# Kernel optimization log

Measured on AMD Instinct MI355X. Metric: run time of the kernel, lower is better.

The kernel has to match this reference:

```python
import jax, jax.numpy as jnp
import numpy as np

N = 20000      # total nodes across the mini-batch of graphs
E = 320000     # edges (avg degree 16)
B = 16         # graphs in the batch
HEADS = 8
EPS_BN = 1e-5
NEG_SLOPE = 0.2


def _lin(k, fan_in, fan_out):
    return (jax.random.normal(k, (fan_in, fan_out), jnp.float32) / np.float32(np.sqrt(fan_in)))


def setup_inputs() -> dict:
    key = jax.random.key(0)
    ks = jax.random.split(key, 24)
    inp = {}
    inp["x"] = jax.random.normal(ks[0], (N, 3), jnp.float32)
    inp["edge_index"] = jax.random.randint(ks[1], (2, E), 0, N, dtype=jnp.int32)
    inp["batch"] = jnp.sort(jax.random.randint(ks[2], (N,), 0, B, dtype=jnp.int32))
    # GATConv params: lin weight [in, heads*out], att_src/att_dst [heads,out], bias [heads*out]
    dims = [(3, 16), (128, 32), (256, 64)]
    for i, (cin, cout) in enumerate(dims, start=1):
        base = 3 + 5 * i
        inp[f"W{i}"] = _lin(ks[base], cin, HEADS * cout)
        inp[f"as{i}"] = jax.random.normal(ks[base + 1], (HEADS, cout), jnp.float32) * 0.1
        inp[f"ad{i}"] = jax.random.normal(ks[base + 2], (HEADS, cout), jnp.float32) * 0.1
        inp[f"b{i}"] = jnp.zeros((HEADS * cout,), jnp.float32)
        inp[f"g{i}"] = jnp.ones((HEADS * cout,), jnp.float32)
        inp[f"be{i}"] = jnp.zeros((HEADS * cout,), jnp.float32)
    inp["fcW"] = _lin(ks[20], 512, 10)
    inp["fcb"] = jnp.zeros((10,), jnp.float32)
    return inp


def gat_layer(x, src, dst, W, a_s, a_d, bias, heads, out_ch):
    n = x.shape[0]
    h = (x @ W).reshape(n, heads, out_ch)              # [N,H,C]
    al_s = jnp.einsum('nhc,hc->nh', h, a_s)            # [N,H]
    al_d = jnp.einsum('nhc,hc->nh', h, a_d)
    e = jax.nn.leaky_relu(al_s[src] + al_d[dst], NEG_SLOPE)   # [E,H]
    m = jax.ops.segment_max(e, dst, num_segments=n)    # per-dst softmax (stable)
    e = jnp.exp(e - m[dst])
    denom = jax.ops.segment_sum(e, dst, num_segments=n)
    alpha = e / (denom[dst] + 1e-16)
    out = jax.ops.segment_sum(h[src] * alpha[:, :, None], dst, num_segments=n)
    return out.reshape(n, heads * out_ch) + bias


def bn_relu(x, g, b):
    mu = x.mean(0)
    var = x.var(0)  # biased, as torch BN uses for normalization
    return jax.nn.relu((x - mu) * jax.lax.rsqrt(var + EPS_BN) * g + b)


def reference(x, edge_index, batch, W1, as1, ad1, b1, g1, be1,
              W2, as2, ad2, b2, g2, be2, W3, as3, ad3, b3, g3, be3, fcW, fcb):
    n = x.shape[0]
    loops = jnp.arange(n, dtype=edge_index.dtype)
    src = jnp.concatenate([edge_index[0], loops])  # add_self_loops=True (PyG default)
    dst = jnp.concatenate([edge_index[1], loops])
    h = bn_relu(gat_layer(x, src, dst, W1, as1, ad1, b1, HEADS, 16), g1, be1)
    h = bn_relu(gat_layer(h, src, dst, W2, as2, ad2, b2, HEADS, 32), g2, be2)
    h = bn_relu(gat_layer(h, src, dst, W3, as3, ad3, b3, HEADS, 64), g3, be3)
    pooled = jax.ops.segment_max(h, batch, num_segments=B)  # global_max_pool
    return pooled @ fcW + fcb
```

## Files before the change

### kernel.cpp

```cpp
#include <hip/hip_runtime.h>
#include <hip/hip_bf16.h>

#define HEADS 8
#define EPS_BN 1e-5f
#define NEG_SLOPE 0.2f
#define BN_NB 256

typedef __attribute__((ext_vector_type(8))) short bf16x8;
typedef __attribute__((ext_vector_type(4))) float f32x4;

__device__ __forceinline__ float bf2f(unsigned short u) {
    return __uint_as_float(((unsigned int)u) << 16);
}

__device__ __forceinline__ unsigned short f2bf(float f) {
    __hip_bfloat16 b = __float2bfloat16(f);
    return *reinterpret_cast<unsigned short*>(&b);
}

__device__ __forceinline__ void gld_lds16(const ushort* g, ushort* l) {
    __builtin_amdgcn_global_load_lds(
        (const __attribute__((address_space(1))) unsigned int*)g,
        (__attribute__((address_space(3))) unsigned int*)l, 16, 0, 0);
}


__global__ void count_kernel(const int* __restrict__ ei, int E, int N, int* __restrict__ counts) {
    int i = blockIdx.x * blockDim.x + threadIdx.x;
    int total = E + N;
    if (i >= total) return;
    int d = (i < E) ? ei[E + i] : (i - E);
    atomicAdd(&counts[d], 1);
}

__global__ __launch_bounds__(1024) void scan_block_kernel(const int* __restrict__ counts,
                                                          int* __restrict__ offs,
                                                          int* __restrict__ part, int n) {
    __shared__ int tile[1024];
    int tid = threadIdx.x;
    int gid = blockIdx.x * 1024 + tid;
    int v = (gid < n) ? counts[gid] : 0;
    tile[tid] = v;
    __syncthreads();
    for (int off = 1; off < 1024; off <<= 1) {
        int t = (tid >= off) ? tile[tid - off] : 0;
        __syncthreads();
        tile[tid] += t;
        __syncthreads();
    }
    if (gid < n) offs[gid + 1] = tile[tid];
    if (tid == 1023) part[blockIdx.x] = tile[1023];
}

__global__ __launch_bounds__(1024) void scan_add_kernel(int* __restrict__ offs,
                                                        const int* __restrict__ part, int n) {
    __shared__ int base;
    if (threadIdx.x == 0) {
        int s = 0;
        for (int i = 0; i < (int)blockIdx.x; ++i) s += part[i];
        base = s;
    }
    __syncthreads();
    int gid = blockIdx.x * 1024 + threadIdx.x;
    if (gid < n) offs[gid + 1] += base;
    if (gid == 0) offs[0] = 0;
}

__global__ void scatter_kernel(const int* __restrict__ ei, int E, int N,
                               const int* __restrict__ offs, int* __restrict__ cursor,
                               int* __restrict__ csr_src) {
    int i = blockIdx.x * blockDim.x + threadIdx.x;
    int total = E + N;
    if (i >= total) return;
    int s, d;
    if (i < E) { s = ei[i]; d = ei[E + i]; } else { s = i - E; d = i - E; }
    int slot = atomicAdd(&cursor[d], 1);
    csr_src[offs[d] + slot] = s;
}


__global__ __launch_bounds__(256) void linear1_al_kernel(const float* __restrict__ x,
                                                         const float* __restrict__ W,
                                                         const float* __restrict__ a_s,
                                                         const float* __restrict__ a_d,
                                                         ushort* __restrict__ h,
                                                         float* __restrict__ als,
                                                         float* __restrict__ ald, int N) {
    int tid = threadIdx.x;
    int n = blockIdx.x * 2 + (tid >> 7);
    int f = tid & 127;
    if (n >= N) return;
    float acc = x[n * 3 + 0] * W[f] + x[n * 3 + 1] * W[128 + f] + x[n * 3 + 2] * W[256 + f];
    h[(size_t)n * 128 + f] = f2bf(acc);
    float s = acc * a_s[f];
    float ds = acc * a_d[f];
    s += __shfl_xor(s, 1);  ds += __shfl_xor(ds, 1);
    s += __shfl_xor(s, 2);  ds += __shfl_xor(ds, 2);
    s += __shfl_xor(s, 4);  ds += __shfl_xor(ds, 4);
    s += __shfl_xor(s, 8);  ds += __shfl_xor(ds, 8);
    if ((f & 15) == 0) {
        int head = f >> 4;
        als[n * 8 + head] = s;
        ald[n * 8 + head] = ds;
    }
}


__global__ __launch_bounds__(256) void transpose_both_kernel(const float* __restrict__ W2,
                                                             ushort* __restrict__ Wt2,
                                                             const float* __restrict__ W3,
                                                             ushort* __restrict__ Wt3) {
    __shared__ float t[32][33];
    int bid = blockIdx.x;
    const float* W; ushort* Wt; int K, Nc, b;
    if (bid < 32) { W = W2; Wt = Wt2; K = 128; Nc = 256; b = bid; }
    else          { W = W3; Wt = Wt3; K = 256; Nc = 512; b = bid - 32; }
    int nb = Nc / 32;
    int bx = b % nb, by = b / nb;
    int n0 = bx * 32, k0 = by * 32;
    int lx = threadIdx.x & 31, ly = threadIdx.x >> 5;
    for (int r = ly; r < 32; r += 8) t[r][lx] = W[(size_t)(k0 + r) * Nc + n0 + lx];
    __syncthreads();
    for (int r = ly; r < 32; r += 8) Wt[(size_t)(n0 + r) * K + k0 + lx] = f2bf(t[lx][r]);
}


template<int F>
__global__ void prep_kernel(const ushort4* __restrict__ xb, const float* __restrict__ scale,
                            const float* __restrict__ shift, ushort4* __restrict__ A, int n4) {
    int i = blockIdx.x * blockDim.x + threadIdx.x;
    if (i >= n4) return;
    ushort4 u = xb[i];
    int f = (i << 2) & (F - 1);
    float4 sc = *(const float4*)(scale + f);
    float4 sh = *(const float4*)(shift + f);
    ushort4 o;
    o.x = f2bf(fmaxf(bf2f(u.x) * sc.x + sh.x, 0.f));
    o.y = f2bf(fmaxf(bf2f(u.y) * sc.y + sh.y, 0.f));
    o.z = f2bf(fmaxf(bf2f(u.z) * sc.z + sh.z, 0.f));
    o.w = f2bf(fmaxf(bf2f(u.w) * sc.w + sh.w, 0.f));
    A[i] = o;
}


template<int K, int C>
__global__ __launch_bounds__(256) void mfma_gemm_kernel(const ushort* __restrict__ A,
                                                        const ushort* __restrict__ Bt,
                                                        ushort* __restrict__ Cout,
                                                        const float* __restrict__ a_s,
                                                        const float* __restrict__ a_d,
                                                        float* __restrict__ als,
                                                        float* __restrict__ ald,
                                                        int M, int Ncols) {
    __shared__ __align__(16) ushort lA[128 * 64];
    __shared__ __align__(16) ushort lB[128 * 64];
    int tid = threadIdx.x;
    int l = tid & 63, w = tid >> 6;
    int m0 = blockIdx.x * 128;
    int n0 = blockIdx.y * 128;
    int wm = w >> 1, wn = w & 1;
    f32x4 zero = {0.f, 0.f, 0.f, 0.f};
    f32x4 acc[4][4];
#pragma unroll
    for (int m = 0; m < 4; ++m)
#pragma unroll
        for (int n = 0; n < 4; ++n) acc[m][n] = zero;

#pragma unroll
    for (int k0 = 0; k0 < K; k0 += 64) {
        if (k0) __syncthreads();
#pragma unroll
        for (int i = 0; i < 4; ++i) {
            int idx = (w * 4 + i) * 64 + l;
            int row = idx >> 3, p = idx & 7;
            int gc = (p ^ (row & 7)) * 8;
            int ar = m0 + row; ar = (ar < M) ? ar : (M - 1);
            gld_lds16(A + (size_t)ar * K + k0 + gc, &lA[idx * 8]);
            gld_lds16(Bt + (size_t)(n0 + row) * K + k0 + gc, &lB[idx * 8]);
        }
        __syncthreads();
#pragma unroll
        for (int ks = 0; ks < 2; ++ks) {
            bf16x8 af[4], bfr[4];
#pragma unroll
            for (int m = 0; m < 4; ++m) {
                int row = wm * 64 + m * 16 + (l & 15);
                int cp = (ks * 4 + (l >> 4)) ^ (row & 7);
                af[m] = *(const bf16x8*)&lA[row * 64 + cp * 8];
            }
#pragma unroll
            for (int n = 0; n < 4; ++n) {
                int row = wn * 64 + n * 16 + (l & 15);
                int cp = (ks * 4 + (l >> 4)) ^ (row & 7);
                bfr[n] = *(const bf16x8*)&lB[row * 64 + cp * 8];
            }
#pragma unroll
            for (int m = 0; m < 4; ++m)
#pragma unroll
                for (int n = 0; n < 4; ++n)
                    acc[m][n] = __builtin_amdgcn_mfma_f32_16x16x32_bf16(af[m], bfr[n], acc[m][n], 0, 0, 0);
        }
    }
    int lr = (l >> 4) * 4, lc = l & 15;
#pragma unroll
    for (int m = 0; m < 4; ++m) {
#pragma unroll
        for (int q = 0; q < 4; ++q) {
            int r = m0 + wm * 64 + m * 16 + lr + q;
            if (r < M) {
#pragma unroll
                for (int n = 0; n < 4; ++n) {
                    int c = n0 + wn * 64 + n * 16 + lc;
                    Cout[(size_t)r * Ncols + c] = f2bf(acc[m][n][q]);
                }
            }
        }
    }
    constexpr int GRP = (C == 64) ? 4 : 2;
    constexpr int NGRP = 4 / GRP;
    float asv[4], adv[4];
#pragma unroll
    for (int n = 0; n < 4; ++n) {
        int cc = n0 + wn * 64 + n * 16 + lc;
        asv[n] = a_s[cc];
        adv[n] = a_d[cc];
    }
#pragma unroll
    for (int m = 0; m < 4; ++m) {
#pragma unroll
        for (int q = 0; q < 4; ++q) {
            int r = m0 + wm * 64 + m * 16 + lr + q;
#pragma unroll
            for (int gg = 0; gg < NGRP; ++gg) {
                float s = 0.f, ds = 0.f;
#pragma unroll
                for (int nn = 0; nn < GRP; ++nn) {
                    int n = gg * GRP + nn;
                    s += acc[m][n][q] * asv[n];
                    ds += acc[m][n][q] * adv[n];
                }
                s += __shfl_xor(s, 1);  ds += __shfl_xor(ds, 1);
                s += __shfl_xor(s, 2);  ds += __shfl_xor(ds, 2);
                s += __shfl_xor(s, 4);  ds += __shfl_xor(ds, 4);
                s += __shfl_xor(s, 8);  ds += __shfl_xor(ds, 8);
                if (lc == 0 && r < M) {
                    int head = (n0 + wn * 64 + gg * (GRP * 16)) / C;
                    als[r * 8 + head] = s;
                    ald[r * 8 + head] = ds;
                }
            }
        }
    }
}


template<int CPL>
__device__ __forceinline__ void gather_accum(const ushort* hp, float wt, float* acc) {
    unsigned int u[CPL / 2];
    if constexpr (CPL == 8) {
        uint4 v = *(const uint4*)hp; u[0] = v.x; u[1] = v.y; u[2] = v.z; u[3] = v.w;
    } else if constexpr (CPL == 4) {
        uint2 v = *(const uint2*)hp; u[0] = v.x; u[1] = v.y;
    } else {
        u[0] = *(const unsigned int*)hp;
    }
#pragma unroll
    for (int j = 0; j < CPL / 2; ++j) {
        acc[2 * j]     += wt * __uint_as_float(u[j] << 16);
        acc[2 * j + 1] += wt * __uint_as_float(u[j] & 0xffff0000u);
    }
}

template<int F, int C>
__global__ __launch_bounds__(256) void aggregate_kernel(const ushort* __restrict__ h,
                                                        const float* __restrict__ als,
                                                        const float* __restrict__ ald,
                                                        const int* __restrict__ offs,
                                                        const int* __restrict__ csr_src,
                                                        const float* __restrict__ bias,
                                                        ushort* __restrict__ outbf, int N) {
    constexpr int CPL = F / 64;
    int w = threadIdx.x >> 6, l = threadIdx.x & 63;
    int d = blockIdx.x * 4 + w;
    if (d >= N) return;
    int start = offs[d];
    int deg = offs[d + 1] - start;
    int hf = l >> 3;
    int hw = l & 7;
    int jslot = l >> 3;
    float aldw = ald[d * 8 + hw];

    float acc[CPL];
#pragma unroll
    for (int j = 0; j < CPL; ++j) acc[j] = 0.f;
    float dsum = 0.f;
    float mrun = -1e30f;

    int nfull = deg & ~7;
    for (int eb = 0; eb < nfull; eb += 8) {
        int sE = (l < 8) ? csr_src[start + eb + l] : 0;
        int smy = __shfl(sE, jslot);
        float v = als[smy * 8 + hw] + aldw;
        v = (v > 0.f) ? v : NEG_SLOPE * v;
        float bm = v;
        bm = fmaxf(bm, __shfl_xor(bm, 8));
        bm = fmaxf(bm, __shfl_xor(bm, 16));
        bm = fmaxf(bm, __shfl_xor(bm, 32));
        float mnew = fmaxf(mrun, bm);
        float rs = __expf(mrun - mnew);
        float pw = __expf(v - mnew);
        dsum = dsum * rs + pw;
        float rsg = __shfl(rs, hf);
#pragma unroll
        for (int j = 0; j < CPL; ++j) acc[j] *= rsg;
        mrun = mnew;
#pragma unroll
        for (int j = 0; j < 8; ++j) {
            int sj = __shfl(sE, j);
            float wt = __shfl(pw, (j << 3) + hf);
            gather_accum<CPL>(h + (size_t)sj * F + l * CPL, wt, acc);
        }
    }
    int rem = deg - nfull;
    if (rem) {
        int sE = (l < rem) ? csr_src[start + nfull + l] : 0;
        int smy = __shfl(sE, jslot);
        float v = -1e30f;
        if (jslot < rem) {
            v = als[smy * 8 + hw] + aldw;
            v = (v > 0.f) ? v : NEG_SLOPE * v;
        }
        float bm = v;
        bm = fmaxf(bm, __shfl_xor(bm, 8));
        bm = fmaxf(bm, __shfl_xor(bm, 16));
        bm = fmaxf(bm, __shfl_xor(bm, 32));
        float mnew = fmaxf(mrun, bm);
        float rs = __expf(mrun - mnew);
        float pw = __expf(v - mnew);
        dsum = dsum * rs + pw;
        float rsg = __shfl(rs, hf);
#pragma unroll
        for (int j = 0; j < CPL; ++j) acc[j] *= rsg;
        for (int j = 0; j < rem; ++j) {
            int sj = __shfl(sE, j);
            float wt = __shfl(pw, (j << 3) + hf);
            gather_accum<CPL>(h + (size_t)sj * F + l * CPL, wt, acc);
        }
    }
    dsum += __shfl_xor(dsum, 8);
    dsum += __shfl_xor(dsum, 16);
    dsum += __shfl_xor(dsum, 32);
    float den = __shfl(dsum, hf);
    float inv = 1.0f / (den + 1e-16f);
    int cbase = l * CPL;
#pragma unroll
    for (int j = 0; j < CPL; ++j)
        outbf[(size_t)d * F + cbase + j] = f2bf(acc[j] * inv + bias[cbase + j]);
}


template<int F>
__global__ __launch_bounds__(256) void bnA_kernel(const ushort* __restrict__ xb,
                                                  float* __restrict__ part,
                                                  int N, int npb) {
    constexpr int F4 = F / 4;
    constexpr int RPI = 256 / F4;
    __shared__ float sdata[256 * 8];
    int tid = threadIdx.x;
    int c4 = tid % F4;
    int ro = tid / F4;
    int n0 = blockIdx.x * npb;
    int n1 = n0 + npb;
    if (n1 > N) n1 = N;
    float s0 = 0, s1 = 0, s2 = 0, s3 = 0, q0 = 0, q1 = 0, q2 = 0, q3 = 0;
    for (int r = n0 + ro; r < n1; r += RPI) {
        ushort4 u = *(const ushort4*)(xb + (size_t)r * F + c4 * 4);
        float v0 = bf2f(u.x), v1 = bf2f(u.y), v2 = bf2f(u.z), v3 = bf2f(u.w);
        s0 += v0; s1 += v1; s2 += v2; s3 += v3;
        q0 += v0 * v0; q1 += v1 * v1; q2 += v2 * v2; q3 += v3 * v3;
    }
    float* sp = &sdata[tid * 8];
    sp[0] = s0; sp[1] = s1; sp[2] = s2; sp[3] = s3;
    sp[4] = q0; sp[5] = q1; sp[6] = q2; sp[7] = q3;
    __syncthreads();
    if (tid < F4) {
        float t[8];
#pragma unroll
        for (int k = 0; k < 8; ++k) t[k] = sdata[tid * 8 + k];
        for (int j = 1; j < RPI; ++j) {
            const float* op = &sdata[(j * F4 + tid) * 8];
#pragma unroll
            for (int k = 0; k < 8; ++k) t[k] += op[k];
        }
        float* pb = part + (size_t)blockIdx.x * 2 * F;
#pragma unroll
        for (int k = 0; k < 4; ++k) {
            pb[tid * 4 + k]     = t[k];
            pb[F + tid * 4 + k] = t[4 + k];
        }
    }
}

template<int F>
__global__ void bnB_kernel(const float* __restrict__ part,
                           const float* __restrict__ g, const float* __restrict__ be,
                           float* __restrict__ scale, float* __restrict__ shift, int N) {
    int f = blockIdx.x * blockDim.x + threadIdx.x;
    if (f >= F) return;
    float sum = 0.f, sq = 0.f;
#pragma unroll 4
    for (int j = 0; j < BN_NB; ++j) {
        sum += part[(size_t)j * 2 * F + f];
        sq  += part[(size_t)j * 2 * F + F + f];
    }
    float invN = 1.0f / (float)N;
    float mean = sum * invN;
    float var = sq * invN - mean * mean;
    float sc = g[f] * rsqrtf(var + EPS_BN);
    scale[f] = sc;
    shift[f] = be[f] - mean * sc;
}


__global__ __launch_bounds__(256) void poolA_kernel(const ushort* __restrict__ xb,
                                                    const int* __restrict__ batch,
                                                    const float* __restrict__ scale,
                                                    const float* __restrict__ shift,
                                                    float* __restrict__ pooled8, int N) {
    int tid = threadIdx.x;
    int c4 = tid & 127;
    int ro = tid >> 7;
    int n0 = blockIdx.x * 64;
    int n1 = n0 + 64;
    if (n1 > N) n1 = N;
    float4 sc = ((const float4*)scale)[c4];
    float4 sh = ((const float4*)shift)[c4];
    float* pbase = pooled8 + (size_t)(blockIdx.x & 7) * (16 * 512);
    float m0 = 0.f, m1 = 0.f, m2 = 0.f, m3 = 0.f;
    int cur = -1;
    for (int n = n0 + ro; n < n1; n += 2) {
        int b = batch[n];
        if (b != cur) {
            if (cur >= 0) {
                int base = cur * 512 + c4 * 4;
                atomicMax((int*)&pbase[base],     __float_as_int(m0));
                atomicMax((int*)&pbase[base + 1], __float_as_int(m1));
                atomicMax((int*)&pbase[base + 2], __float_as_int(m2));
                atomicMax((int*)&pbase[base + 3], __float_as_int(m3));
            }
            cur = b;
            m0 = m1 = m2 = m3 = 0.f;
        }
        ushort4 u = *(const ushort4*)(xb + (size_t)n * 512 + c4 * 4);
        m0 = fmaxf(m0, bf2f(u.x) * sc.x + sh.x);
        m1 = fmaxf(m1, bf2f(u.y) * sc.y + sh.y);
        m2 = fmaxf(m2, bf2f(u.z) * sc.z + sh.z);
        m3 = fmaxf(m3, bf2f(u.w) * sc.w + sh.w);
    }
    if (cur >= 0) {
        int base = cur * 512 + c4 * 4;
        atomicMax((int*)&pbase[base],     __float_as_int(m0));
        atomicMax((int*)&pbase[base + 1], __float_as_int(m1));
        atomicMax((int*)&pbase[base + 2], __float_as_int(m2));
        atomicMax((int*)&pbase[base + 3], __float_as_int(m3));
    }
}

__global__ __launch_bounds__(512) void poolFC_kernel(const float* __restrict__ pooled8,
                                                     const float* __restrict__ fcW,
                                                     const float* __restrict__ fcb,
                                                     float* __restrict__ out) {
    __shared__ float sp[16 * 513];
    __shared__ float sw[512 * 10];
    int tid = threadIdx.x;
    for (int c = tid; c < 16 * 512; c += 512) {
        float m = pooled8[c];
#pragma unroll
        for (int k = 1; k < 8; ++k) m = fmaxf(m, pooled8[k * 16 * 512 + c]);
        int b = c >> 9, f = c & 511;
        sp[b * 513 + f] = m;
    }
    for (int i = tid; i < 512 * 10; i += 512) sw[i] = fcW[i];
    __syncthreads();
    if (tid < 160) {
        int b = tid / 10, j = tid % 10;
        float acc = fcb[j];
        const float* spb = &sp[b * 513];
#pragma unroll 8
        for (int f = 0; f < 512; ++f) acc += spb[f] * sw[f * 10 + j];
        out[tid] = acc;
    }
}


extern "C" void kernel_launch(void* const* d_in, const int* in_sizes, int n_in,
                              void* d_out, int out_size, void* d_ws, size_t ws_size,
                              hipStream_t stream) {
    const float* x   = (const float*)d_in[0];
    const int* ei    = (const int*)d_in[1];
    const int* batch = (const int*)d_in[2];
    const float* W1  = (const float*)d_in[3];
    const float* as1 = (const float*)d_in[4];
    const float* ad1 = (const float*)d_in[5];
    const float* b1  = (const float*)d_in[6];
    const float* g1  = (const float*)d_in[7];
    const float* be1 = (const float*)d_in[8];
    const float* W2  = (const float*)d_in[9];
    const float* as2 = (const float*)d_in[10];
    const float* ad2 = (const float*)d_in[11];
    const float* b2  = (const float*)d_in[12];
    const float* g2  = (const float*)d_in[13];
    const float* be2 = (const float*)d_in[14];
    const float* W3  = (const float*)d_in[15];
    const float* as3 = (const float*)d_in[16];
    const float* ad3 = (const float*)d_in[17];
    const float* b3  = (const float*)d_in[18];
    const float* g3  = (const float*)d_in[19];
    const float* be3 = (const float*)d_in[20];
    const float* fcW = (const float*)d_in[21];
    const float* fcb = (const float*)d_in[22];
    float* out = (float*)d_out;

    int N = in_sizes[0] / 3;
    int E = in_sizes[1] / 2;

    char* p = (char*)d_ws;
    auto alloc = [&](size_t bytes) {
        char* r = p;
        p += (bytes + 255) & ~(size_t)255;
        return r;
    };
    char* zbase   = p;
    int*   counts = (int*)alloc((size_t)N * 4);
    int*   cursor = (int*)alloc((size_t)N * 4);
    float* pooled8 = (float*)alloc(8 * 16 * 512 * 4);
    size_t zbytes = (size_t)(p - zbase);
    int*   offs   = (int*)alloc((size_t)(N + 1) * 4);
    int*   part   = (int*)alloc(64 * 4);
    int*   csr    = (int*)alloc((size_t)(E + N) * 4);
    ushort* h     = (ushort*)alloc((size_t)N * 512 * 2);
    ushort* aggbf = (ushort*)alloc((size_t)N * 512 * 2);
    ushort* Abuf  = (ushort*)alloc((size_t)N * 512 * 2);
    ushort* Wt2   = (ushort*)alloc(256 * 128 * 2);
    ushort* Wt3   = (ushort*)alloc(512 * 256 * 2);
    float* als    = (float*)alloc((size_t)N * 8 * 4);
    float* ald    = (float*)alloc((size_t)N * 8 * 4);
    float* bnpart = (float*)alloc((size_t)BN_NB * 1024 * 4);
    float* scale  = (float*)alloc(512 * 4);
    float* shift  = (float*)alloc(512 * 4);

    int total_e = E + N;
    int nchunks = (N + 1023) / 1024;
    int mtiles = (N + 127) / 128;
    int bnnpb = (N + BN_NB - 1) / BN_NB;
    int ablocks = (N + 3) / 4;
    int pblocks = (N + 63) / 64;

    hipMemsetAsync(zbase, 0, zbytes, stream);

    count_kernel<<<(total_e + 255) / 256, 256, 0, stream>>>(ei, E, N, counts);
    scan_block_kernel<<<nchunks, 1024, 0, stream>>>(counts, offs, part, N);
    scan_add_kernel<<<nchunks, 1024, 0, stream>>>(offs, part, N);
    scatter_kernel<<<(total_e + 255) / 256, 256, 0, stream>>>(ei, E, N, offs, cursor, csr);

    transpose_both_kernel<<<160, 256, 0, stream>>>(W2, Wt2, W3, Wt3);

    linear1_al_kernel<<<(N + 1) / 2, 256, 0, stream>>>(x, W1, as1, ad1, h, als, ald, N);
    aggregate_kernel<128, 16><<<ablocks, 256, 0, stream>>>(h, als, ald, offs, csr, b1, aggbf, N);
    bnA_kernel<128><<<BN_NB, 256, 0, stream>>>(aggbf, bnpart, N, bnnpb);
    bnB_kernel<128><<<1, 128, 0, stream>>>(bnpart, g1, be1, scale, shift, N);

    prep_kernel<128><<<(N * 128 / 4 + 255) / 256, 256, 0, stream>>>(
        (const ushort4*)aggbf, scale, shift, (ushort4*)Abuf, N * 128 / 4);
    mfma_gemm_kernel<128, 32><<<dim3(mtiles, 2), 256, 0, stream>>>(
        Abuf, Wt2, h, as2, ad2, als, ald, N, 256);
    aggregate_kernel<256, 32><<<ablocks, 256, 0, stream>>>(h, als, ald, offs, csr, b2, aggbf, N);
    bnA_kernel<256><<<BN_NB, 256, 0, stream>>>(aggbf, bnpart, N, bnnpb);
    bnB_kernel<256><<<1, 256, 0, stream>>>(bnpart, g2, be2, scale, shift, N);

    prep_kernel<256><<<(N * 256 / 4 + 255) / 256, 256, 0, stream>>>(
        (const ushort4*)aggbf, scale, shift, (ushort4*)Abuf, N * 256 / 4);
    mfma_gemm_kernel<256, 64><<<dim3(mtiles, 4), 256, 0, stream>>>(
        Abuf, Wt3, h, as3, ad3, als, ald, N, 512);
    aggregate_kernel<512, 64><<<ablocks, 256, 0, stream>>>(h, als, ald, offs, csr, b3, aggbf, N);
    bnA_kernel<512><<<BN_NB, 256, 0, stream>>>(aggbf, bnpart, N, bnnpb);
    bnB_kernel<512><<<2, 256, 0, stream>>>(bnpart, g3, be3, scale, shift, N);

    poolA_kernel<<<pblocks, 256, 0, stream>>>(aggbf, batch, scale, shift, pooled8, N);
    poolFC_kernel<<<1, 512, 0, stream>>>(pooled8, fcW, fcb, out);
}
```

Baseline: 325.3 us.

## Fuse BN-apply into GEMM, merge small kernels via last-block reductions

Removes the separate prep kernels by applying the BN scale/shift and ReLU while loading the A tile in the GEMM, so the Abuf round-trip through memory goes away. The two-pass scan becomes a single-block scan. The weight transpose is folded into the layer-1 linear kernel, and the bnB and poolFC kernels are merged into their predecessors through an atomic last-block-done counter. Together these cut about eight kernel launches and one full activation write and read per layer. The cost is that the GEMM now stages A through registers instead of async global-to-LDS loads, and the serial scan and last-block tails run on a single block.

```diff
diff --git a/kernel.cpp b/kernel.cpp
--- a/kernel.cpp
+++ b/kernel.cpp
@@ -33,37 +33,26 @@
     atomicAdd(&counts[d], 1);
 }
 
-__global__ __launch_bounds__(1024) void scan_block_kernel(const int* __restrict__ counts,
-                                                          int* __restrict__ offs,
-                                                          int* __restrict__ part, int n) {
+__global__ __launch_bounds__(1024) void scan_kernel(const int* __restrict__ counts,
+                                                    int* __restrict__ offs, int n) {
     __shared__ int tile[1024];
     int tid = threadIdx.x;
-    int gid = blockIdx.x * 1024 + tid;
-    int v = (gid < n) ? counts[gid] : 0;
-    tile[tid] = v;
-    __syncthreads();
-    for (int off = 1; off < 1024; off <<= 1) {
-        int t = (tid >= off) ? tile[tid - off] : 0;
+    int carry = 0;
+    for (int base = 0; base < n; base += 1024) {
+        int v = (base + tid < n) ? counts[base + tid] : 0;
+        tile[tid] = v;
         __syncthreads();
-        tile[tid] += t;
+        for (int off = 1; off < 1024; off <<= 1) {
+            int t = (tid >= off) ? tile[tid - off] : 0;
+            __syncthreads();
+            tile[tid] += t;
+            __syncthreads();
+        }
+        if (base + tid < n) offs[base + tid + 1] = carry + tile[tid];
+        carry += tile[1023];
         __syncthreads();
     }
-    if (gid < n) offs[gid + 1] = tile[tid];
-    if (tid == 1023) part[blockIdx.x] = tile[1023];
-}
-
-__global__ __launch_bounds__(1024) void scan_add_kernel(int* __restrict__ offs,
-                                                        const int* __restrict__ part, int n) {
-    __shared__ int base;
-    if (threadIdx.x == 0) {
-        int s = 0;
-        for (int i = 0; i < (int)blockIdx.x; ++i) s += part[i];
-        base = s;
-    }
-    __syncthreads();
-    int gid = blockIdx.x * 1024 + threadIdx.x;
-    if (gid < n) offs[gid + 1] += base;
-    if (gid == 0) offs[0] = 0;
+    if (tid == 0) offs[0] = 0;
 }
 
 __global__ void scatter_kernel(const int* __restrict__ ei, int E, int N,
@@ -79,15 +68,33 @@
 }
 
 
-__global__ __launch_bounds__(256) void linear1_al_kernel(const float* __restrict__ x,
-                                                         const float* __restrict__ W,
-                                                         const float* __restrict__ a_s,
-                                                         const float* __restrict__ a_d,
-                                                         ushort* __restrict__ h,
-                                                         float* __restrict__ als,
-                                                         float* __restrict__ ald, int N) {
+__global__ __launch_bounds__(256) void linear1_al_tr_kernel(const float* __restrict__ x,
+                                                            const float* __restrict__ W,
+                                                            const float* __restrict__ a_s,
+                                                            const float* __restrict__ a_d,
+                                                            ushort* __restrict__ h,
+                                                            float* __restrict__ als,
+                                                            float* __restrict__ ald, int N,
+                                                            const float* __restrict__ W2,
+                                                            ushort* __restrict__ Wt2,
+                                                            const float* __restrict__ W3,
+                                                            ushort* __restrict__ Wt3) {
+    __shared__ float t[32][33];
     int tid = threadIdx.x;
-    int n = blockIdx.x * 2 + (tid >> 7);
+    int bid = blockIdx.x;
+    if (bid < 160) {
+        const float* Ws; ushort* Wt; int K, Nc, b;
+        if (bid < 32) { Ws = W2; Wt = Wt2; K = 128; Nc = 256; b = bid; }
+        else          { Ws = W3; Wt = Wt3; K = 256; Nc = 512; b = bid - 32; }
+        int nb = Nc / 32;
+        int bx = b % nb, by = b / nb;
+        int n0 = bx * 32, k0 = by * 32;
+        int lx = tid & 31, ly = tid >> 5;
+        for (int r = ly; r < 32; r += 8) t[r][lx] = Ws[(size_t)(k0 + r) * Nc + n0 + lx];
+        __syncthreads();
+        for (int r = ly; r < 32; r += 8) Wt[(size_t)(n0 + r) * K + k0 + lx] = f2bf(t[lx][r]);
+    }
+    int n = bid * 2 + (tid >> 7);
     int f = tid & 127;
     if (n >= N) return;
     float acc = x[n * 3 + 0] * W[f] + x[n * 3 + 1] * W[128 + f] + x[n * 3 + 2] * W[256 + f];
@@ -106,45 +113,10 @@
 }
 
 
-__global__ __launch_bounds__(256) void transpose_both_kernel(const float* __restrict__ W2,
-                                                             ushort* __restrict__ Wt2,
-                                                             const float* __restrict__ W3,
-                                                             ushort* __restrict__ Wt3) {
-    __shared__ float t[32][33];
-    int bid = blockIdx.x;
-    const float* W; ushort* Wt; int K, Nc, b;
-    if (bid < 32) { W = W2; Wt = Wt2; K = 128; Nc = 256; b = bid; }
-    else          { W = W3; Wt = Wt3; K = 256; Nc = 512; b = bid - 32; }
-    int nb = Nc / 32;
-    int bx = b % nb, by = b / nb;
-    int n0 = bx * 32, k0 = by * 32;
-    int lx = threadIdx.x & 31, ly = threadIdx.x >> 5;
-    for (int r = ly; r < 32; r += 8) t[r][lx] = W[(size_t)(k0 + r) * Nc + n0 + lx];
-    __syncthreads();
-    for (int r = ly; r < 32; r += 8) Wt[(size_t)(n0 + r) * K + k0 + lx] = f2bf(t[lx][r]);
-}
-
-
-template<int F>
-__global__ void prep_kernel(const ushort4* __restrict__ xb, const float* __restrict__ scale,
-                            const float* __restrict__ shift, ushort4* __restrict__ A, int n4) {
-    int i = blockIdx.x * blockDim.x + threadIdx.x;
-    if (i >= n4) return;
-    ushort4 u = xb[i];
-    int f = (i << 2) & (F - 1);
-    float4 sc = *(const float4*)(scale + f);
-    float4 sh = *(const float4*)(shift + f);
-    ushort4 o;
-    o.x = f2bf(fmaxf(bf2f(u.x) * sc.x + sh.x, 0.f));
-    o.y = f2bf(fmaxf(bf2f(u.y) * sc.y + sh.y, 0.f));
-    o.z = f2bf(fmaxf(bf2f(u.z) * sc.z + sh.z, 0.f));
-    o.w = f2bf(fmaxf(bf2f(u.w) * sc.w + sh.w, 0.f));
-    A[i] = o;
-}
-
-
 template<int K, int C>
 __global__ __launch_bounds__(256) void mfma_gemm_kernel(const ushort* __restrict__ A,
+                                                        const float* __restrict__ scale,
+                                                        const float* __restrict__ shift,
                                                         const ushort* __restrict__ Bt,
                                                         ushort* __restrict__ Cout,
                                                         const float* __restrict__ a_s,
@@ -174,9 +146,37 @@
             int idx = (w * 4 + i) * 64 + l;
             int row = idx >> 3, p = idx & 7;
             int gc = (p ^ (row & 7)) * 8;
+            gld_lds16(Bt + (size_t)(n0 + row) * K + k0 + gc, &lB[idx * 8]);
+        }
+#pragma unroll
+        for (int i = 0; i < 4; ++i) {
+            int idx = (w * 4 + i) * 64 + l;
+            int row = idx >> 3, p = idx & 7;
+            int gc = (p ^ (row & 7)) * 8;
             int ar = m0 + row; ar = (ar < M) ? ar : (M - 1);
-            gld_lds16(A + (size_t)ar * K + k0 + gc, &lA[idx * 8]);
-            gld_lds16(Bt + (size_t)(n0 + row) * K + k0 + gc, &lB[idx * 8]);
+            int kk = k0 + gc;
+            uint4 raw = *(const uint4*)(A + (size_t)ar * K + kk);
+            float4 sc0 = *(const float4*)(scale + kk);
+            float4 sc1 = *(const float4*)(scale + kk + 4);
+            float4 sh0 = *(const float4*)(shift + kk);
+            float4 sh1 = *(const float4*)(shift + kk + 4);
+            unsigned int rr0 = raw.x, rr1 = raw.y, rr2 = raw.z, rr3 = raw.w;
+            float v0, v1;
+            unsigned int o0, o1, o2, o3;
+            v0 = fmaxf(__uint_as_float(rr0 << 16) * sc0.x + sh0.x, 0.f);
+            v1 = fmaxf(__uint_as_float(rr0 & 0xffff0000u) * sc0.y + sh0.y, 0.f);
+            o0 = (unsigned int)f2bf(v0) | ((unsigned int)f2bf(v1) << 16);
+            v0 = fmaxf(__uint_as_float(rr1 << 16) * sc0.z + sh0.z, 0.f);
+            v1 = fmaxf(__uint_as_float(rr1 & 0xffff0000u) * sc0.w + sh0.w, 0.f);
+            o1 = (unsigned int)f2bf(v0) | ((unsigned int)f2bf(v1) << 16);
+            v0 = fmaxf(__uint_as_float(rr2 << 16) * sc1.x + sh1.x, 0.f);
+            v1 = fmaxf(__uint_as_float(rr2 & 0xffff0000u) * sc1.y + sh1.y, 0.f);
+            o2 = (unsigned int)f2bf(v0) | ((unsigned int)f2bf(v1) << 16);
+            v0 = fmaxf(__uint_as_float(rr3 << 16) * sc1.z + sh1.z, 0.f);
+            v1 = fmaxf(__uint_as_float(rr3 & 0xffff0000u) * sc1.w + sh1.w, 0.f);
+            o3 = (unsigned int)f2bf(v0) | ((unsigned int)f2bf(v1) << 16);
+            uint4 pk = {o0, o1, o2, o3};
+            *(uint4*)&lA[idx * 8] = pk;
         }
         __syncthreads();
 #pragma unroll
@@ -360,9 +360,14 @@
 
 
 template<int F>
-__global__ __launch_bounds__(256) void bnA_kernel(const ushort* __restrict__ xb,
-                                                  float* __restrict__ part,
-                                                  int N, int npb) {
+__global__ __launch_bounds__(256) void bnAB_kernel(const ushort* __restrict__ xb,
+                                                   float* __restrict__ part,
+                                                   const float* __restrict__ g,
+                                                   const float* __restrict__ be,
+                                                   float* __restrict__ scale,
+                                                   float* __restrict__ shift,
+                                                   int* __restrict__ ctr,
+                                                   int N, int npb) {
     constexpr int F4 = F / 4;
     constexpr int RPI = 256 / F4;
     __shared__ float sdata[256 * 8];
@@ -399,34 +404,40 @@
             pb[F + tid * 4 + k] = t[4 + k];
         }
     }
-}
-
-template<int F>
-__global__ void bnB_kernel(const float* __restrict__ part,
-                           const float* __restrict__ g, const float* __restrict__ be,
-                           float* __restrict__ scale, float* __restrict__ shift, int N) {
-    int f = blockIdx.x * blockDim.x + threadIdx.x;
-    if (f >= F) return;
-    float sum = 0.f, sq = 0.f;
-#pragma unroll 4
-    for (int j = 0; j < BN_NB; ++j) {
-        sum += part[(size_t)j * 2 * F + f];
-        sq  += part[(size_t)j * 2 * F + F + f];
-    }
-    float invN = 1.0f / (float)N;
-    float mean = sum * invN;
-    float var = sq * invN - mean * mean;
-    float sc = g[f] * rsqrtf(var + EPS_BN);
-    scale[f] = sc;
-    shift[f] = be[f] - mean * sc;
-}
-
-
-__global__ __launch_bounds__(256) void poolA_kernel(const ushort* __restrict__ xb,
-                                                    const int* __restrict__ batch,
-                                                    const float* __restrict__ scale,
-                                                    const float* __restrict__ shift,
-                                                    float* __restrict__ pooled8, int N) {
+    __threadfence();
+    __shared__ int slast;
+    if (tid == 0) slast = (atomicAdd(ctr, 1) == BN_NB - 1) ? 1 : 0;
+    __syncthreads();
+    if (slast) {
+        __threadfence();
+        float invN = 1.0f / (float)N;
+        for (int f = tid; f < F; f += 256) {
+            float sum = 0.f, sq = 0.f;
+            for (int j = 0; j < BN_NB; ++j) {
+                sum += part[(size_t)j * 2 * F + f];
+                sq  += part[(size_t)j * 2 * F + F + f];
+            }
+            float mean = sum * invN;
+            float var = sq * invN - mean * mean;
+            float sc = g[f] * rsqrtf(var + EPS_BN);
+            scale[f] = sc;
+            shift[f] = be[f] - mean * sc;
+        }
+    }
+}
+
+
+__global__ __launch_bounds__(256) void poolAFC_kernel(const ushort* __restrict__ xb,
+                                                      const int* __restrict__ batch,
+                                                      const float* __restrict__ scale,
+                                                      const float* __restrict__ shift,
+                                                      float* __restrict__ pooled8,
+                                                      int* __restrict__ ctr,
+                                                      const float* __restrict__ fcW,
+                                                      const float* __restrict__ fcb,
+                                                      float* __restrict__ out,
+                                                      int N, int nblocks) {
+    __shared__ float sp[16 * 513];
     int tid = threadIdx.x;
     int c4 = tid & 127;
     int ro = tid >> 7;
@@ -464,31 +475,27 @@
         atomicMax((int*)&pbase[base + 2], __float_as_int(m2));
         atomicMax((int*)&pbase[base + 3], __float_as_int(m3));
     }
-}
-
-__global__ __launch_bounds__(512) void poolFC_kernel(const float* __restrict__ pooled8,
-                                                     const float* __restrict__ fcW,
-                                                     const float* __restrict__ fcb,
-                                                     float* __restrict__ out) {
-    __shared__ float sp[16 * 513];
-    __shared__ float sw[512 * 10];
-    int tid = threadIdx.x;
-    for (int c = tid; c < 16 * 512; c += 512) {
-        float m = pooled8[c];
-#pragma unroll
-        for (int k = 1; k < 8; ++k) m = fmaxf(m, pooled8[k * 16 * 512 + c]);
-        int b = c >> 9, f = c & 511;
-        sp[b * 513 + f] = m;
-    }
-    for (int i = tid; i < 512 * 10; i += 512) sw[i] = fcW[i];
+    __threadfence();
+    __shared__ int slast;
+    if (tid == 0) slast = (atomicAdd(ctr, 1) == nblocks - 1) ? 1 : 0;
     __syncthreads();
-    if (tid < 160) {
-        int b = tid / 10, j = tid % 10;
-        float acc = fcb[j];
-        const float* spb = &sp[b * 513];
+    if (slast) {
+        __threadfence();
+        for (int c = tid; c < 16 * 512; c += 256) {
+            float m = pooled8[c];
+#pragma unroll
+            for (int k = 1; k < 8; ++k) m = fmaxf(m, pooled8[k * 16 * 512 + c]);
+            sp[(c >> 9) * 513 + (c & 511)] = m;
+        }
+        __syncthreads();
+        if (tid < 160) {
+            int b = tid / 10, j = tid % 10;
+            float acc = fcb[j];
+            const float* spb = &sp[b * 513];
 #pragma unroll 8
-        for (int f = 0; f < 512; ++f) acc += spb[f] * sw[f * 10 + j];
-        out[tid] = acc;
+            for (int f = 0; f < 512; ++f) acc += spb[f] * fcW[f * 10 + j];
+            out[tid] = acc;
+        }
     }
 }
 
@@ -533,14 +540,13 @@
     char* zbase   = p;
     int*   counts = (int*)alloc((size_t)N * 4);
     int*   cursor = (int*)alloc((size_t)N * 4);
+    int*   ctrs   = (int*)alloc(8 * 4);
     float* pooled8 = (float*)alloc(8 * 16 * 512 * 4);
     size_t zbytes = (size_t)(p - zbase);
     int*   offs   = (int*)alloc((size_t)(N + 1) * 4);
-    int*   part   = (int*)alloc(64 * 4);
     int*   csr    = (int*)alloc((size_t)(E + N) * 4);
     ushort* h     = (ushort*)alloc((size_t)N * 512 * 2);
     ushort* aggbf = (ushort*)alloc((size_t)N * 512 * 2);
-    ushort* Abuf  = (ushort*)alloc((size_t)N * 512 * 2);
     ushort* Wt2   = (ushort*)alloc(256 * 128 * 2);
     ushort* Wt3   = (ushort*)alloc(512 * 256 * 2);
     float* als    = (float*)alloc((size_t)N * 8 * 4);
@@ -550,7 +556,6 @@
     float* shift  = (float*)alloc(512 * 4);
 
     int total_e = E + N;
-    int nchunks = (N + 1023) / 1024;
     int mtiles = (N + 127) / 128;
     int bnnpb = (N + BN_NB - 1) / BN_NB;
     int ablocks = (N + 3) / 4;
@@ -559,33 +564,27 @@
     hipMemsetAsync(zbase, 0, zbytes, stream);
 
     count_kernel<<<(total_e + 255) / 256, 256, 0, stream>>>(ei, E, N, counts);
-    scan_block_kernel<<<nchunks, 1024, 0, stream>>>(counts, offs, part, N);
-    scan_add_kernel<<<nchunks, 1024, 0, stream>>>(offs, part, N);
+    scan_kernel<<<1, 1024, 0, stream>>>(counts, offs, N);
     scatter_kernel<<<(total_e + 255) / 256, 256, 0, stream>>>(ei, E, N, offs, cursor, csr);
 
-    transpose_both_kernel<<<160, 256, 0, stream>>>(W2, Wt2, W3, Wt3);
-
-    linear1_al_kernel<<<(N + 1) / 2, 256, 0, stream>>>(x, W1, as1, ad1, h, als, ald, N);
+    linear1_al_tr_kernel<<<(N + 1) / 2, 256, 0, stream>>>(x, W1, as1, ad1, h, als, ald, N,
+                                                          W2, Wt2, W3, Wt3);
     aggregate_kernel<128, 16><<<ablocks, 256, 0, stream>>>(h, als, ald, offs, csr, b1, aggbf, N);
-    bnA_kernel<128><<<BN_NB, 256, 0, stream>>>(aggbf, bnpart, N, bnnpb);
-    bnB_kernel<128><<<1, 128, 0, stream>>>(bnpart, g1, be1, scale, shift, N);
-
-    prep_kernel<128><<<(N * 128 / 4 + 255) / 256, 256, 0, stream>>>(
-        (const ushort4*)aggbf, scale, shift, (ushort4*)Abuf, N * 128 / 4);
+    bnAB_kernel<128><<<BN_NB, 256, 0, stream>>>(aggbf, bnpart, g1, be1, scale, shift,
+                                                &ctrs[0], N, bnnpb);
+
     mfma_gemm_kernel<128, 32><<<dim3(mtiles, 2), 256, 0, stream>>>(
-        Abuf, Wt2, h, as2, ad2, als, ald, N, 256);
+        aggbf, scale, shift, Wt2, h, as2, ad2, als, ald, N, 256);
     aggregate_kernel<256, 32><<<ablocks, 256, 0, stream>>>(h, als, ald, offs, csr, b2, aggbf, N);
-    bnA_kernel<256><<<BN_NB, 256, 0, stream>>>(aggbf, bnpart, N, bnnpb);
-    bnB_kernel<256><<<1, 256, 0, stream>>>(bnpart, g2, be2, scale, shift, N);
-
-    prep_kernel<256><<<(N * 256 / 4 + 255) / 256, 256, 0, stream>>>(
-        (const ushort4*)aggbf, scale, shift, (ushort4*)Abuf, N * 256 / 4);
+    bnAB_kernel<256><<<BN_NB, 256, 0, stream>>>(aggbf, bnpart, g2, be2, scale, shift,
+                                                &ctrs[1], N, bnnpb);
+
     mfma_gemm_kernel<256, 64><<<dim3(mtiles, 4), 256, 0, stream>>>(
-        Abuf, Wt3, h, as3, ad3, als, ald, N, 512);
+        aggbf, scale, shift, Wt3, h, as3, ad3, als, ald, N, 512);
     aggregate_kernel<512, 64><<<ablocks, 256, 0, stream>>>(h, als, ald, offs, csr, b3, aggbf, N);
-    bnA_kernel<512><<<BN_NB, 256, 0, stream>>>(aggbf, bnpart, N, bnnpb);
-    bnB_kernel<512><<<2, 256, 0, stream>>>(bnpart, g3, be3, scale, shift, N);
-
-    poolA_kernel<<<pblocks, 256, 0, stream>>>(aggbf, batch, scale, shift, pooled8, N);
-    poolFC_kernel<<<1, 512, 0, stream>>>(pooled8, fcW, fcb, out);
-}
+    bnAB_kernel<512><<<BN_NB, 256, 0, stream>>>(aggbf, bnpart, g3, be3, scale, shift,
+                                                &ctrs[2], N, bnnpb);
+
+    poolAFC_kernel<<<pblocks, 256, 0, stream>>>(aggbf, batch, scale, shift, pooled8,
+                                                &ctrs[3], fcW, fcb, out, N, pblocks);
+}
```

New measurement: 413.7 us. 27.2% more time.
